# Performance work log

Hardware: AMD Instinct MI355X
Metric: run time of the kernel (lower is better)

The kernel has to match this reference:

```python
import jax, jax.numpy as jnp
import numpy as np

DIM = 180; HEADS = 6; WS = 8; CONV_SCALE = 0.01
B = 4; H = 256; W = 256

def _rpi(ws):
    coords = np.stack(np.meshgrid(np.arange(ws), np.arange(ws), indexing='ij')).reshape(2, -1)
    rel = (coords[:, :, None] - coords[:, None, :]).transpose(1, 2, 0)
    rel[:, :, 0] += ws - 1; rel[:, :, 1] += ws - 1
    rel[:, :, 0] *= 2 * ws - 1
    return rel.sum(-1)  # (ws*ws, ws*ws)

def setup_inputs():
    ks = jax.random.split(jax.random.key(0), 10)
    d = DIM
    n = lambda i, shape: jax.random.normal(ks[i], shape, jnp.float32) * 0.02
    return {
        'x': jax.random.normal(ks[0], (B, H * W, d), jnp.float32),
        'ln1_g': jnp.ones((d,), jnp.float32), 'ln1_b': jnp.zeros((d,), jnp.float32),
        'qkv_w': n(1, (3 * d, d)), 'qkv_b': jnp.zeros((3 * d,), jnp.float32),
        'bias_table': n(2, ((2 * WS - 1) ** 2, HEADS)),
        'proj_w': n(3, (d, d)), 'proj_b': jnp.zeros((d,), jnp.float32),
        'cab_w1': n(4, (d // 3, d, 3, 3)), 'cab_b1': jnp.zeros((d // 3,), jnp.float32),
        'cab_w2': n(5, (d, d // 3, 3, 3)), 'cab_b2': jnp.zeros((d,), jnp.float32),
        'ca_w1': n(6, (d // 30, d, 1, 1)), 'ca_b1': jnp.zeros((d // 30,), jnp.float32),
        'ca_w2': n(7, (d, d // 30, 1, 1)), 'ca_b2': jnp.zeros((d,), jnp.float32),
        'ln2_g': jnp.ones((d,), jnp.float32), 'ln2_b': jnp.zeros((d,), jnp.float32),
        'fc1_w': n(8, (4 * d, d)), 'fc1_b': jnp.zeros((4 * d,), jnp.float32),
        'fc2_w': n(9, (d, 4 * d)), 'fc2_b': jnp.zeros((d,), jnp.float32),
        'rpi': jnp.asarray(_rpi(WS), jnp.int32),
        'h': H, 'w': W,
    }

def _ln(x, g, b, eps=1e-5):
    m = x.mean(-1, keepdims=True)
    v = ((x - m) ** 2).mean(-1, keepdims=True)
    return (x - m) / jnp.sqrt(v + eps) * g + b

def _conv(x, w, b, pad):
    y = jax.lax.conv_general_dilated(x, w, (1, 1), [(pad, pad), (pad, pad)],
                                     dimension_numbers=('NCHW', 'OIHW', 'NCHW'))
    return y + b[None, :, None, None]

def _hab(x, ln1_g, ln1_b, qkv_w, qkv_b, bias_table, proj_w, proj_b,
         cab_w1, cab_b1, cab_w2, cab_b2, ca_w1, ca_b1, ca_w2, ca_b2,
         ln2_g, ln2_b, fc1_w, fc1_b, fc2_w, fc2_b, rpi, h, w):
    b, _, c = x.shape
    ws, heads = WS, HEADS
    hd = c // heads
    shortcut = x
    xn = _ln(x, ln1_g, ln1_b).reshape(b, h, w, c)
    # --- CAB conv branch ---
    xc = xn.transpose(0, 3, 1, 2)  # NCHW
    y = jax.nn.gelu(_conv(xc, cab_w1, cab_b1, 1), approximate=False)
    y = _conv(y, cab_w2, cab_b2, 1)
    a = y.mean((2, 3), keepdims=True)  # adaptive avg pool to 1x1
    a = jax.nn.relu(_conv(a, ca_w1, ca_b1, 0))
    a = jax.nn.sigmoid(_conv(a, ca_w2, ca_b2, 0))
    conv_x = (y * a).transpose(0, 2, 3, 1).reshape(b, h * w, c)
    # --- window attention (shift_size = 0, no mask) ---
    nwin_tok = ws * ws
    xw = xn.reshape(b, h // ws, ws, w // ws, ws, c).transpose(0, 1, 3, 2, 4, 5).reshape(-1, nwin_tok, c)
    qkv = (xw @ qkv_w.T + qkv_b).reshape(-1, nwin_tok, 3, heads, hd).transpose(2, 0, 3, 1, 4)
    q, k, v = qkv[0] * (hd ** -0.5), qkv[1], qkv[2]
    attn = jnp.einsum('whnd,whmd->whnm', q, k)  # (nW*b, heads, n, n)
    bias = bias_table[rpi.reshape(-1)].reshape(nwin_tok, nwin_tok, heads).transpose(2, 0, 1)
    attn = jax.nn.softmax(attn + bias[None], axis=-1)
    out = jnp.einsum('whnm,whmd->whnd', attn, v).transpose(0, 2, 1, 3).reshape(-1, nwin_tok, c)
    out = out @ proj_w.T + proj_b
    attn_x = out.reshape(b, h // ws, w // ws, ws, ws, c).transpose(0, 1, 3, 2, 4, 5).reshape(b, h * w, c)
    x = shortcut + attn_x + conv_x * CONV_SCALE
    x = x + (jax.nn.gelu(_ln(x, ln2_g, ln2_b) @ fc1_w.T + fc1_b, approximate=False) @ fc2_w.T + fc2_b)
    return x

def reference(x, ln1_g, ln1_b, qkv_w, qkv_b, bias_table, proj_w, proj_b,
              cab_w1, cab_b1, cab_w2, cab_b2, ca_w1, ca_b1, ca_w2, ca_b2,
              ln2_g, ln2_b, fc1_w, fc1_b, fc2_w, fc2_b, rpi, h, w):
    return _hab(x, ln1_g, ln1_b, qkv_w, qkv_b, bias_table, proj_w, proj_b,
                cab_w1, cab_b1, cab_w2, cab_b2, ca_w1, ca_b1, ca_w2, ca_b2,
                ln2_g, ln2_b, fc1_w, fc1_b, fc2_w, fc2_b, rpi, h, w)
```

## Files before the change

kernel.cpp:

```cpp
#include <hip/hip_runtime.h>
#include <hip/hip_bf16.h>

typedef __hip_bfloat16 bf16;
typedef __attribute__((ext_vector_type(8))) short short8v;
typedef __attribute__((ext_vector_type(4))) float float4v;

#define N_TOK (4 * 65536)
#define IMG 256

__device__ __forceinline__ float wave_reduce_add(float v) {
#pragma unroll
  for (int m = 32; m > 0; m >>= 1) v += __shfl_xor(v, m, 64);
  return v;
}

__device__ __forceinline__ float gelu_f(float v) {
  return 0.5f * v * (1.f + erff(v * 0.70710678118654752f));
}

__device__ __forceinline__ size_t frag_idx(long row, int k) {
  return ((((row >> 6) * 24) + (k >> 3)) << 9) + ((long)(row & 63) << 3) + (k & 7);
}


__global__ void k_zero(float* __restrict__ p, int n) {
  int i = blockIdx.x * 256 + threadIdx.x;
  if (i < n) p[i] = 0.f;
}

__global__ void k_pack_qkv_b(const float* __restrict__ w, bf16* __restrict__ B) {
  int e = blockIdx.x * 256 + threadIdx.x;
  if (e >= 34 * 6 * 64) return;
  int lane = e & 63, kb = (e >> 6) % 6, nt = e / (6 * 64);
  int n = nt * 16 + (lane & 15);
  int kbase = kb * 32 + (lane >> 4) * 8;
  bf16* out = B + (size_t)e * 8;
#pragma unroll
  for (int j = 0; j < 8; j++) {
    int k = kbase + j;
    float v = 0.f;
    if (n < 540 && k < 180) {
      int hh = n / 90, r = n % 90, mat = r / 30, d = r % 30;
      int o = mat * 180 + hh * 30 + d;
      float s = (mat == 0) ? 0.18257418583505537f : 1.f;
      v = w[o * 180 + k] * s;
    }
    out[j] = __float2bfloat16(v);
  }
}

__global__ void k_pack_qkv_bias(const float* __restrict__ b, float* __restrict__ bt) {
  int n = blockIdx.x * 256 + threadIdx.x;
  if (n >= 544) return;
  float v = 0.f;
  if (n < 540) {
    int hh = n / 90, r = n % 90, mat = r / 30, d = r % 30;
    int o = mat * 180 + hh * 30 + d;
    float s = (mat == 0) ? 0.18257418583505537f : 1.f;
    v = b[o] * s;
  }
  bt[n] = v;
}

__global__ void k_pack_proj_b(const float* __restrict__ w, bf16* __restrict__ B) {
  int e = blockIdx.x * 256 + threadIdx.x;
  if (e >= 12 * 6 * 64) return;
  int lane = e & 63, kb = (e >> 6) % 6, nt = e / (6 * 64);
  int n = nt * 16 + (lane & 15);
  int kbase = kb * 32 + (lane >> 4) * 8;
  bf16* out = B + (size_t)e * 8;
#pragma unroll
  for (int j = 0; j < 8; j++) {
    int k = kbase + j;
    out[j] = __float2bfloat16((n < 180 && k < 180) ? w[n * 180 + k] : 0.f);
  }
}

__global__ void k_pack_fc1_b(const float* __restrict__ w, bf16* __restrict__ B) {
  int e = blockIdx.x * 256 + threadIdx.x;
  if (e >= 46 * 6 * 64) return;
  int lane = e & 63, kb = (e >> 6) % 6, nt = e / (6 * 64);
  int n = nt * 16 + (lane & 15);
  int kbase = kb * 32 + (lane >> 4) * 8;
  bf16* out = B + (size_t)e * 8;
#pragma unroll
  for (int j = 0; j < 8; j++) {
    int k = kbase + j;
    out[j] = __float2bfloat16((n < 720 && k < 180) ? w[n * 180 + k] : 0.f);
  }
}

__global__ void k_pack_fc1_bias(const float* __restrict__ b, float* __restrict__ bt) {
  int n = blockIdx.x * 256 + threadIdx.x;
  if (n >= 736) return;
  bt[n] = (n < 720) ? b[n] : 0.f;
}

__global__ void k_pack_fc2_b(const float* __restrict__ w, bf16* __restrict__ B) {
  int e = blockIdx.x * 256 + threadIdx.x;
  if (e >= 12 * 23 * 64) return;
  int lane = e & 63, kb = (e >> 6) % 23, nt = e / (23 * 64);
  int n = nt * 16 + (lane & 15);
  int kbase = kb * 32 + (lane >> 4) * 8;
  bf16* out = B + (size_t)e * 8;
#pragma unroll
  for (int j = 0; j < 8; j++) {
    int k = kbase + j;
    out[j] = __float2bfloat16((n < 180 && k < 720) ? w[n * 720 + k] : 0.f);
  }
}

__global__ void k_pack_conv1_b(const float* __restrict__ w, bf16* __restrict__ B) {
  int e = blockIdx.x * 256 + threadIdx.x;
  if (e >= 9 * 6 * 4 * 64) return;
  int lane = e & 63;
  int t = e >> 6;
  int nt = t & 3;
  int t2 = t >> 2;
  int dx = t2 % 3;
  int t3 = t2 / 3;
  int kb = t3 % 6, dy = t3 / 6;
  int n = nt * 16 + (lane & 15);
  int kbase = kb * 32 + (lane >> 4) * 8;
  bf16* out = B + (size_t)e * 8;
#pragma unroll
  for (int j = 0; j < 8; j++) {
    int k = kbase + j;
    float v = (n < 60 && k < 180) ? w[((n * 180 + k) * 3 + dy) * 3 + dx] : 0.f;
    out[j] = __float2bfloat16(v);
  }
}

__global__ void k_pack_conv2_b(const float* __restrict__ w, bf16* __restrict__ B) {
  int e = blockIdx.x * 256 + threadIdx.x;
  if (e >= 9 * 2 * 12 * 64) return;
  int lane = e & 63;
  int t = e >> 6;
  int nt = t % 12;
  int t2 = t / 12;
  int dx = t2 % 3;
  int t3 = t2 / 3;
  int kb = t3 & 1, dy = t3 >> 1;
  int n = nt * 16 + (lane & 15);
  int kbase = kb * 32 + (lane >> 4) * 8;
  bf16* out = B + (size_t)e * 8;
#pragma unroll
  for (int j = 0; j < 8; j++) {
    int k = kbase + j;
    float v = (n < 180 && k < 60) ? w[((n * 60 + k) * 3 + dy) * 3 + dx] : 0.f;
    out[j] = __float2bfloat16(v);
  }
}


__global__ __launch_bounds__(256) void k_ln1(const float* __restrict__ x,
                                             const float* __restrict__ gw,
                                             const float* __restrict__ bw,
                                             bf16* __restrict__ xnf) {
  int wv = threadIdx.x >> 6, lane = threadIdx.x & 63;
  long row = (long)blockIdx.x * 4 + wv;
  const float* xr = x + row * 180;
  float v0 = xr[lane];
  float v1 = xr[lane + 64];
  float v2 = (lane < 52) ? xr[lane + 128] : 0.f;
  float s = wave_reduce_add(v0 + v1 + v2);
  float ss = wave_reduce_add(v0 * v0 + v1 * v1 + v2 * v2);
  float mean = s * (1.f / 180.f);
  float rstd = rsqrtf(ss * (1.f / 180.f) - mean * mean + 1e-5f);
  bf16* base = xnf + (((row >> 6) * 24) << 9) + ((long)(row & 63) << 3);
  int ch = lane >> 3, j = lane & 7;
  base[((size_t)ch << 9) + j] =
      __float2bfloat16((v0 - mean) * rstd * gw[lane] + bw[lane]);
  base[((size_t)(ch + 8) << 9) + j] =
      __float2bfloat16((v1 - mean) * rstd * gw[lane + 64] + bw[lane + 64]);
  float v3 = (lane < 52) ? ((v2 - mean) * rstd * gw[lane + 128] + bw[lane + 128]) : 0.f;
  base[((size_t)(ch + 16) << 9) + j] = __float2bfloat16(v3);
}


__global__ __launch_bounds__(256) void k_conv1_mfma(const bf16* __restrict__ xnf,
                                                    const bf16* __restrict__ Bc1,
                                                    const float* __restrict__ b1,
                                                    bf16* __restrict__ y60f) {
  __shared__ bf16 Ls[3 * 12 * 66 * 8];
  int tid = threadIdx.x;
  int bid = blockIdx.x;
  int b = bid >> 10, rem = bid & 1023, iy = rem >> 2, xb = rem & 3;
  int ix0 = xb << 6;
  long ibase = (long)b * 65536;
  int lane = tid & 63, wv = tid >> 6;
  int m = lane & 15, q = lane >> 4;
  float4v acc[4];
#pragma unroll
  for (int nt = 0; nt < 4; nt++) acc[nt] = (float4v){0.f, 0.f, 0.f, 0.f};
  const short8v* Bp = (const short8v*)Bc1;
  for (int half = 0; half < 2; half++) {
    for (int idx = tid; idx < 3 * 12 * 66; idx += 256) {
      int px = idx % 66;
      int t2 = idx / 66;
      int chb = t2 % 12, r = t2 / 12;
      int iy2 = iy - 1 + r, ix = ix0 - 1 + px;
      uint4 v = make_uint4(0u, 0u, 0u, 0u);
      if (iy2 >= 0 && iy2 < IMG && ix >= 0 && ix < IMG) {
        long tok = ibase + iy2 * IMG + ix;
        v = *(const uint4*)(xnf + ((tok >> 6) * 24 + half * 12 + chb) * 512 +
                            (tok & 63) * 8);
      }
      *(uint4*)(Ls + (size_t)idx * 8) = v;
    }
    __syncthreads();
#pragma unroll
    for (int kbl = 0; kbl < 3; kbl++) {
      int kb = half * 3 + kbl;
#pragma unroll
      for (int dy = 0; dy < 3; dy++) {
        const short8v* ab =
            (const short8v*)Ls + ((dy * 12 + kbl * 4 + q) * 66 + wv * 16 + m);
#pragma unroll
        for (int dx = 0; dx < 3; dx++) {
          short8v a = ab[dx];
          const short8v* bp = Bp + (size_t)(((dy * 6 + kb) * 3 + dx) * 4) * 64 + lane;
#pragma unroll
          for (int nt = 0; nt < 4; nt++)
            acc[nt] = __builtin_amdgcn_mfma_f32_16x16x32_bf16(a, bp[nt * 64], acc[nt], 0, 0, 0);
        }
      }
    }
    __syncthreads();
  }
  bf16* outb = y60f + (size_t)bid * 4096;
#pragma unroll
  for (int nt = 0; nt < 4; nt++) {
    int n = nt * 16 + m;
    float bias = (n < 60) ? b1[n] : 0.f;
#pragma unroll
    for (int reg = 0; reg < 4; reg++) {
      int p = wv * 16 + q * 4 + reg;
      float v = (n < 60) ? gelu_f(acc[nt][reg] + bias) : 0.f;
      outb[((n >> 3) << 9) + (p << 3) + (n & 7)] = __float2bfloat16(v);
    }
  }
}


__global__ __launch_bounds__(256) void k_conv2_mfma(const bf16* __restrict__ y60f,
                                                    const bf16* __restrict__ Bc2,
                                                    const float* __restrict__ b2,
                                                    bf16* __restrict__ y180f,
                                                    float* __restrict__ chsum) {
  __shared__ bf16 Ls[3 * 8 * 66 * 8];
  int tid = threadIdx.x;
  int bid = blockIdx.x;
  int b = bid >> 10, rem = bid & 1023, iy = rem >> 2, xb = rem & 3;
  int ix0 = xb << 6;
  long ibase = (long)b * 65536;
  for (int idx = tid; idx < 3 * 8 * 66; idx += 256) {
    int px = idx % 66;
    int t2 = idx / 66;
    int chb = t2 % 8, r = t2 / 8;
    int iy2 = iy - 1 + r, ix = ix0 - 1 + px;
    uint4 v = make_uint4(0u, 0u, 0u, 0u);
    if (iy2 >= 0 && iy2 < IMG && ix >= 0 && ix < IMG) {
      long tok = ibase + iy2 * IMG + ix;
      v = *(const uint4*)(y60f + ((tok >> 6) * 8 + chb) * 512 + (tok & 63) * 8);
    }
    *(uint4*)(Ls + (size_t)idx * 8) = v;
  }
  __syncthreads();
  int lane = tid & 63, wv = tid >> 6;
  int m = lane & 15, q = lane >> 4;
  float4v acc[12];
#pragma unroll
  for (int nt = 0; nt < 12; nt++) acc[nt] = (float4v){0.f, 0.f, 0.f, 0.f};
  const short8v* Bp = (const short8v*)Bc2;
#pragma unroll
  for (int dy = 0; dy < 3; dy++) {
#pragma unroll
    for (int kb = 0; kb < 2; kb++) {
      const short8v* ab =
          (const short8v*)Ls + ((dy * 8 + kb * 4 + q) * 66 + wv * 16 + m);
#pragma unroll
      for (int dx = 0; dx < 3; dx++) {
        short8v a = ab[dx];
        const short8v* bp = Bp + (size_t)(((dy * 2 + kb) * 3 + dx) * 12) * 64 + lane;
#pragma unroll
        for (int nt = 0; nt < 12; nt++)
          acc[nt] = __builtin_amdgcn_mfma_f32_16x16x32_bf16(a, bp[nt * 64], acc[nt], 0, 0, 0);
      }
    }
  }
  float csum[12];
  bf16* outb = y180f + (size_t)bid * 12288;
#pragma unroll
  for (int nt = 0; nt < 12; nt++) {
    int n = nt * 16 + m;
    float bias = (n < 180) ? b2[n] : 0.f;
    float s = 0.f;
#pragma unroll
    for (int reg = 0; reg < 4; reg++) {
      float v = acc[nt][reg] + bias;
      s += v;
      int p = wv * 16 + q * 4 + reg;
      if (n < 180) outb[((n >> 3) << 9) + (p << 3) + (n & 7)] = __float2bfloat16(v);
    }
    s += __shfl_xor(s, 16, 64);
    s += __shfl_xor(s, 32, 64);
    csum[nt] = s;
  }
  __syncthreads();
  float* red = (float*)Ls;
  if (q == 0) {
#pragma unroll
    for (int nt = 0; nt < 12; nt++) red[wv * 192 + nt * 16 + m] = csum[nt];
  }
  __syncthreads();
  if (tid < 180) {
    float tot = red[tid] + red[192 + tid] + red[384 + tid] + red[576 + tid];
    atomicAdd(&chsum[b * 180 + tid], tot);
  }
}


__global__ __launch_bounds__(192) void k_se(const float* __restrict__ cs,
                                            const float* __restrict__ w1,
                                            const float* __restrict__ b1,
                                            const float* __restrict__ w2,
                                            const float* __restrict__ b2,
                                            float* __restrict__ a_se) {
  __shared__ float m[180];
  __shared__ float hid[6];
  int b = blockIdx.x, t = threadIdx.x;
  if (t < 180) m[t] = cs[b * 180 + t] * (1.f / 65536.f);
  __syncthreads();
  if (t < 6) {
    float s = b1[t];
    for (int c = 0; c < 180; c++) s += m[c] * w1[t * 180 + c];
    hid[t] = fmaxf(s, 0.f);
  }
  __syncthreads();
  if (t < 180) {
    float s = b2[t];
#pragma unroll
    for (int j = 0; j < 6; j++) s += hid[j] * w2[t * 6 + j];
    a_se[b * 180 + t] = 1.f / (1.f + __expf(-s));
  }
}


__global__ __launch_bounds__(256) void k_qkv_mfma(const bf16* __restrict__ xnf,
                                                  const bf16* __restrict__ Bq,
                                                  const float* __restrict__ btq,
                                                  bf16* __restrict__ qkvb) {
  __shared__ bf16 As[24 * 64 * 8];
  int tid = threadIdx.x;
  const uint4* src = (const uint4*)(xnf + (size_t)blockIdx.x * 12288);
  uint4* dst = (uint4*)As;
#pragma unroll
  for (int it = 0; it < 6; it++) dst[it * 256 + tid] = src[it * 256 + tid];
  __syncthreads();
  int lane = tid & 63, wv = tid >> 6;
  int m = lane & 15, q = lane >> 4;
  long row0 = (long)blockIdx.x * 64 + wv * 16;
  const short8v* Ap = (const short8v*)As;
  const short8v* Bp = (const short8v*)Bq;
  for (int nt = 0; nt < 34; nt += 2) {
    float4v acc0 = {0.f, 0.f, 0.f, 0.f}, acc1 = {0.f, 0.f, 0.f, 0.f};
#pragma unroll
    for (int kb = 0; kb < 6; kb++) {
      short8v a = Ap[(kb * 4 + q) * 64 + wv * 16 + m];
      short8v b0 = Bp[(nt * 6 + kb) * 64 + lane];
      short8v b1 = Bp[((nt + 1) * 6 + kb) * 64 + lane];
      acc0 = __builtin_amdgcn_mfma_f32_16x16x32_bf16(a, b0, acc0, 0, 0, 0);
      acc1 = __builtin_amdgcn_mfma_f32_16x16x32_bf16(a, b1, acc1, 0, 0, 0);
    }
    int n0 = nt * 16 + m, n1 = n0 + 16;
    float bb0 = btq[n0], bb1 = btq[n1];
#pragma unroll
    for (int reg = 0; reg < 4; reg++) {
      long rw = row0 + q * 4 + reg;
      qkvb[rw * 544 + n0] = __float2bfloat16(acc0[reg] + bb0);
      qkvb[rw * 544 + n1] = __float2bfloat16(acc1[reg] + bb1);
    }
  }
}


__global__ __launch_bounds__(256) void k_attn(const bf16* __restrict__ qkvb,
                                              const float* __restrict__ btab,
                                              const int* __restrict__ rpi,
                                              bf16* __restrict__ attnf) {
  __shared__ float qkvh[90 * 65];
  __shared__ float sT[64 * 65];
  int h = blockIdx.y;
  int bid = blockIdx.x;
  int b = bid >> 10, rem = bid & 1023, wi = rem >> 5, wj = rem & 31;
  long ibase = (long)b * 65536;
  if (h == 0 && threadIdx.x < 64) {
    int n = threadIdx.x;
    long g = ibase + (wi * 8 + (n >> 3)) * IMG + wj * 8 + (n & 7);
    bf16* bp = attnf + (((g >> 6) * 24) << 9) + ((long)(g & 63) << 3);
    *(uint2*)(bp + (22 << 9) + 4) = make_uint2(0u, 0u);
    *(uint4*)(bp + (23 << 9)) = make_uint4(0u, 0u, 0u, 0u);
  }
  for (int idx = threadIdx.x; idx < 64 * 90; idx += 256) {
    int t = idx / 90, r = idx % 90;
    long g = ibase + (wi * 8 + (t >> 3)) * IMG + wj * 8 + (t & 7);
    qkvh[r * 65 + t] = __bfloat162float(qkvb[g * 544 + h * 90 + r]);
  }
  __syncthreads();
  {
    int m = threadIdx.x & 63, ng = threadIdx.x >> 6;
    int n0 = ng * 16;
    float acc[16];
#pragma unroll
    for (int j = 0; j < 16; j++) acc[j] = 0.f;
    for (int d = 0; d < 30; d++) {
      float kv = qkvh[(30 + d) * 65 + m];
      const float* qp = qkvh + d * 65 + n0;
#pragma unroll
      for (int j = 0; j < 16; j++) acc[j] += kv * qp[j];
    }
#pragma unroll
    for (int j = 0; j < 16; j++) {
      int n = n0 + j;
      sT[m * 65 + n] = acc[j] + btab[rpi[n * 64 + m] * 6 + h];
    }
  }
  __syncthreads();
  if (threadIdx.x < 64) {
    int n = threadIdx.x;
    float mx = -1e30f;
    for (int m2 = 0; m2 < 64; m2++) mx = fmaxf(mx, sT[m2 * 65 + n]);
    float s = 0.f;
    for (int m2 = 0; m2 < 64; m2++) {
      float e = __expf(sT[m2 * 65 + n] - mx);
      sT[m2 * 65 + n] = e;
      s += e;
    }
    float inv = 1.f / s;
    for (int m2 = 0; m2 < 64; m2++) sT[m2 * 65 + n] *= inv;
  }
  __syncthreads();
  for (int it = threadIdx.x; it < 120; it += 256) {
    int d = it % 30, ng = it / 30;
    int n0 = ng * 16;
    float acc[16];
#pragma unroll
    for (int j = 0; j < 16; j++) acc[j] = 0.f;
    for (int m2 = 0; m2 < 64; m2++) {
      float vv = qkvh[(60 + d) * 65 + m2];
      const float* pp = sT + m2 * 65 + n0;
#pragma unroll
      for (int j = 0; j < 16; j++) acc[j] += vv * pp[j];
    }
    int k = h * 30 + d;
#pragma unroll
    for (int j = 0; j < 16; j++) {
      int n = n0 + j;
      long g = ibase + (wi * 8 + (n >> 3)) * IMG + wj * 8 + (n & 7);
      attnf[frag_idx(g, k)] = __float2bfloat16(acc[j]);
    }
  }
}


__global__ __launch_bounds__(256) void k_proj_mfma(const bf16* __restrict__ attnf,
                                                   const bf16* __restrict__ Bp_,
                                                   const float* __restrict__ pb,
                                                   const float* __restrict__ x0,
                                                   const bf16* __restrict__ y180f,
                                                   const float* __restrict__ a_se,
                                                   float* __restrict__ out) {
  __shared__ bf16 As[24 * 64 * 8];
  int tid = threadIdx.x;
  const uint4* src = (const uint4*)(attnf + (size_t)blockIdx.x * 12288);
  uint4* dst = (uint4*)As;
#pragma unroll
  for (int it = 0; it < 6; it++) dst[it * 256 + tid] = src[it * 256 + tid];
  __syncthreads();
  int lane = tid & 63, wv = tid >> 6;
  int m = lane & 15, q = lane >> 4;
  long row0 = (long)blockIdx.x * 64 + wv * 16;
  const short8v* Ap = (const short8v*)As;
  const short8v* Bpp = (const short8v*)Bp_;
  for (int nt = 0; nt < 12; nt += 2) {
    float4v acc0 = {0.f, 0.f, 0.f, 0.f}, acc1 = {0.f, 0.f, 0.f, 0.f};
#pragma unroll
    for (int kb = 0; kb < 6; kb++) {
      short8v a = Ap[(kb * 4 + q) * 64 + wv * 16 + m];
      short8v b0 = Bpp[(nt * 6 + kb) * 64 + lane];
      short8v b1 = Bpp[((nt + 1) * 6 + kb) * 64 + lane];
      acc0 = __builtin_amdgcn_mfma_f32_16x16x32_bf16(a, b0, acc0, 0, 0, 0);
      acc1 = __builtin_amdgcn_mfma_f32_16x16x32_bf16(a, b1, acc1, 0, 0, 0);
    }
    int n0 = nt * 16 + m, n1 = n0 + 16;
    float pb0 = pb[n0];
    float pb1 = (n1 < 180) ? pb[n1] : 0.f;
#pragma unroll
    for (int reg = 0; reg < 4; reg++) {
      long rw = row0 + q * 4 + reg;
      int bidx = (int)(rw >> 16);
      long gi0 = rw * 180 + n0;
      out[gi0] = x0[gi0] + acc0[reg] + pb0 +
                 __bfloat162float(y180f[frag_idx(rw, n0)]) * a_se[bidx * 180 + n0] * 0.01f;
      if (n1 < 180) {
        long gi1 = rw * 180 + n1;
        out[gi1] = x0[gi1] + acc1[reg] + pb1 +
                   __bfloat162float(y180f[frag_idx(rw, n1)]) * a_se[bidx * 180 + n1] * 0.01f;
      }
    }
  }
}


__global__ __launch_bounds__(512, 4) void k_mlp_mfma(float* __restrict__ xio,
                                                     const float* __restrict__ gw,
                                                     const float* __restrict__ bw,
                                                     const bf16* __restrict__ B1,
                                                     const float* __restrict__ b1t,
                                                     const bf16* __restrict__ B2,
                                                     const float* __restrict__ fc2b) {
  __shared__ bf16 Axs[32 * 200];
  __shared__ bf16 Hs[32 * 744];
  int tid = threadIdx.x, lane = tid & 63, wv = tid >> 6;
  long row0 = (long)blockIdx.x * 32;
#pragma unroll
  for (int rr = 0; rr < 4; rr++) {
    int r = wv * 4 + rr;
    const float* xr = xio + (row0 + r) * 180;
    float v0 = xr[lane], v1 = xr[lane + 64];
    float v2 = (lane < 52) ? xr[lane + 128] : 0.f;
    float s = wave_reduce_add(v0 + v1 + v2);
    float ss = wave_reduce_add(v0 * v0 + v1 * v1 + v2 * v2);
    float mean = s * (1.f / 180.f);
    float rstd = rsqrtf(ss * (1.f / 180.f) - mean * mean + 1e-5f);
    bf16* ar = Axs + r * 200;
    ar[lane] = __float2bfloat16((v0 - mean) * rstd * gw[lane] + bw[lane]);
    ar[lane + 64] = __float2bfloat16((v1 - mean) * rstd * gw[lane + 64] + bw[lane + 64]);
    float v3 = (lane < 52) ? ((v2 - mean) * rstd * gw[lane + 128] + bw[lane + 128]) : 0.f;
    ar[lane + 128] = __float2bfloat16(v3);
  }
  __syncthreads();
  int m = lane & 15, q = lane >> 4, mh = wv & 1, ng = wv >> 1;
  int rA = mh * 16 + m;
  for (int i = 0; i < 12; i += 2) {
    int nt0 = ng * 12 + i;
    if (nt0 >= 46) break;
    bool two = (nt0 + 1) < 46;
    float4v acc0 = {0.f, 0.f, 0.f, 0.f}, acc1 = {0.f, 0.f, 0.f, 0.f};
#pragma unroll
    for (int kb = 0; kb < 6; kb++) {
      short8v a = *(const short8v*)(Axs + rA * 200 + kb * 32 + q * 8);
      short8v b0 = ((const short8v*)B1)[(nt0 * 6 + kb) * 64 + lane];
      acc0 = __builtin_amdgcn_mfma_f32_16x16x32_bf16(a, b0, acc0, 0, 0, 0);
      if (two) {
        short8v b1 = ((const short8v*)B1)[((nt0 + 1) * 6 + kb) * 64 + lane];
        acc1 = __builtin_amdgcn_mfma_f32_16x16x32_bf16(a, b1, acc1, 0, 0, 0);
      }
    }
    int n0 = nt0 * 16 + m;
    float bb0 = b1t[n0];
    float bb1 = two ? b1t[n0 + 16] : 0.f;
#pragma unroll
    for (int reg = 0; reg < 4; reg++) {
      int r = mh * 16 + q * 4 + reg;
      Hs[r * 744 + n0] = __float2bfloat16(gelu_f(acc0[reg] + bb0));
      if (two) Hs[r * 744 + n0 + 16] = __float2bfloat16(gelu_f(acc1[reg] + bb1));
    }
  }
  __syncthreads();
  for (int i = 0; i < 3; i += 2) {
    int nt0 = ng * 3 + i;
    bool two = (i + 1) < 3;
    float4v acc0 = {0.f, 0.f, 0.f, 0.f}, acc1 = {0.f, 0.f, 0.f, 0.f};
    for (int kb = 0; kb < 23; kb++) {
      short8v a = *(const short8v*)(Hs + rA * 744 + kb * 32 + q * 8);
      short8v b0 = ((const short8v*)B2)[(nt0 * 23 + kb) * 64 + lane];
      acc0 = __builtin_amdgcn_mfma_f32_16x16x32_bf16(a, b0, acc0, 0, 0, 0);
      if (two) {
        short8v b1 = ((const short8v*)B2)[((nt0 + 1) * 23 + kb) * 64 + lane];
        acc1 = __builtin_amdgcn_mfma_f32_16x16x32_bf16(a, b1, acc1, 0, 0, 0);
      }
    }
    int n0 = nt0 * 16 + m, n1 = n0 + 16;
#pragma unroll
    for (int reg = 0; reg < 4; reg++) {
      long rw = row0 + mh * 16 + q * 4 + reg;
      if (n0 < 180) xio[rw * 180 + n0] += acc0[reg] + fc2b[n0];
      if (two && n1 < 180) xio[rw * 180 + n1] += acc1[reg] + fc2b[n1];
    }
  }
}


extern "C" void kernel_launch(void* const* d_in, const int* in_sizes, int n_in,
                              void* d_out, int out_size, void* d_ws, size_t ws_size,
                              hipStream_t stream) {
  const float* x = (const float*)d_in[0];
  const float* ln1g = (const float*)d_in[1];
  const float* ln1b = (const float*)d_in[2];
  const float* qkvw = (const float*)d_in[3];
  const float* qkvbias = (const float*)d_in[4];
  const float* btab = (const float*)d_in[5];
  const float* projw = (const float*)d_in[6];
  const float* projb = (const float*)d_in[7];
  const float* cw1 = (const float*)d_in[8];
  const float* cb1 = (const float*)d_in[9];
  const float* cw2 = (const float*)d_in[10];
  const float* cb2 = (const float*)d_in[11];
  const float* caw1 = (const float*)d_in[12];
  const float* cab1 = (const float*)d_in[13];
  const float* caw2 = (const float*)d_in[14];
  const float* cab2 = (const float*)d_in[15];
  const float* ln2g = (const float*)d_in[16];
  const float* ln2b = (const float*)d_in[17];
  const float* fc1w = (const float*)d_in[18];
  const float* fc1b = (const float*)d_in[19];
  const float* fc2w = (const float*)d_in[20];
  const float* fc2b = (const float*)d_in[21];
  const int* rpi = (const int*)d_in[22];
  float* out = (float*)d_out;

  size_t off = 0;
  char* wsb = (char*)d_ws;
  auto alloc = [&](size_t bytes) -> char* {
    char* p = wsb + off;
    off = (off + bytes + 255) & ~(size_t)255;
    return p;
  };
  bf16* xnf = (bf16*)alloc((size_t)N_TOK * 192 * 2);
  bf16* y60f = (bf16*)alloc((size_t)N_TOK * 64 * 2);
  bf16* y180f = (bf16*)alloc((size_t)N_TOK * 192 * 2);
  bf16* qkvb = (bf16*)alloc((size_t)N_TOK * 544 * 2);
  bf16* Bq = (bf16*)alloc(34 * 6 * 64 * 8 * 2);
  float* btq = (float*)alloc(544 * 4);
  bf16* Bp = (bf16*)alloc(12 * 6 * 64 * 8 * 2);
  bf16* B1 = (bf16*)alloc(46 * 6 * 64 * 8 * 2);
  float* b1t = (float*)alloc(736 * 4);
  bf16* B2 = (bf16*)alloc(12 * 23 * 64 * 8 * 2);
  bf16* Bc1 = (bf16*)alloc(9 * 6 * 4 * 64 * 8 * 2);
  bf16* Bc2 = (bf16*)alloc(9 * 2 * 12 * 64 * 8 * 2);
  float* chsum = (float*)alloc(720 * 4);
  float* a_se = (float*)alloc(720 * 4);
  if (off > ws_size) return;
  bf16* attnf = xnf;

  k_zero<<<3, 256, 0, stream>>>(chsum, 720);
  k_pack_qkv_b<<<51, 256, 0, stream>>>(qkvw, Bq);
  k_pack_qkv_bias<<<3, 256, 0, stream>>>(qkvbias, btq);
  k_pack_proj_b<<<18, 256, 0, stream>>>(projw, Bp);
  k_pack_fc1_b<<<69, 256, 0, stream>>>(fc1w, B1);
  k_pack_fc1_bias<<<3, 256, 0, stream>>>(fc1b, b1t);
  k_pack_fc2_b<<<69, 256, 0, stream>>>(fc2w, B2);
  k_pack_conv1_b<<<54, 256, 0, stream>>>(cw1, Bc1);
  k_pack_conv2_b<<<54, 256, 0, stream>>>(cw2, Bc2);

  k_ln1<<<65536, 256, 0, stream>>>(x, ln1g, ln1b, xnf);
  k_conv1_mfma<<<4096, 256, 0, stream>>>(xnf, Bc1, cb1, y60f);
  k_conv2_mfma<<<4096, 256, 0, stream>>>(y60f, Bc2, cb2, y180f, chsum);
  k_se<<<4, 192, 0, stream>>>(chsum, caw1, cab1, caw2, cab2, a_se);
  k_qkv_mfma<<<4096, 256, 0, stream>>>(xnf, Bq, btq, qkvb);
  k_attn<<<dim3(4096, 6), 256, 0, stream>>>(qkvb, btab, rpi, attnf);
  k_proj_mfma<<<4096, 256, 0, stream>>>(attnf, Bp, projb, x, y180f, a_se, out);
  k_mlp_mfma<<<8192, 512, 0, stream>>>(out, ln2g, ln2b, B1, b1t, B2, fc2b);
}
```

Measured before the change: 2.320 ms.

## Rewrite window attention with bf16 MFMA and pad per-head QKV to 32

```diff
diff --git a/kernel.cpp b/kernel.cpp
--- a/kernel.cpp
+++ b/kernel.cpp
@@ -30,17 +30,17 @@
 
 __global__ void k_pack_qkv_b(const float* __restrict__ w, bf16* __restrict__ B) {
   int e = blockIdx.x * 256 + threadIdx.x;
-  if (e >= 34 * 6 * 64) return;
+  if (e >= 36 * 6 * 64) return;
   int lane = e & 63, kb = (e >> 6) % 6, nt = e / (6 * 64);
   int n = nt * 16 + (lane & 15);
   int kbase = kb * 32 + (lane >> 4) * 8;
   bf16* out = B + (size_t)e * 8;
+  int hh = n / 96, rr = n % 96, mat = rr / 32, d = rr % 32;
 #pragma unroll
   for (int j = 0; j < 8; j++) {
     int k = kbase + j;
     float v = 0.f;
-    if (n < 540 && k < 180) {
-      int hh = n / 90, r = n % 90, mat = r / 30, d = r % 30;
+    if (d < 30 && k < 180) {
       int o = mat * 180 + hh * 30 + d;
       float s = (mat == 0) ? 0.18257418583505537f : 1.f;
       v = w[o * 180 + k] * s;
@@ -51,15 +51,23 @@
 
 __global__ void k_pack_qkv_bias(const float* __restrict__ b, float* __restrict__ bt) {
   int n = blockIdx.x * 256 + threadIdx.x;
-  if (n >= 544) return;
+  if (n >= 576) return;
+  int hh = n / 96, rr = n % 96, mat = rr / 32, d = rr % 32;
   float v = 0.f;
-  if (n < 540) {
-    int hh = n / 90, r = n % 90, mat = r / 30, d = r % 30;
+  if (d < 30) {
     int o = mat * 180 + hh * 30 + d;
     float s = (mat == 0) ? 0.18257418583505537f : 1.f;
     v = b[o] * s;
   }
   bt[n] = v;
+}
+
+__global__ void k_pack_bias6(const float* __restrict__ btab, const int* __restrict__ rpi,
+                             float* __restrict__ bt6) {
+  int e = blockIdx.x * 256 + threadIdx.x;
+  if (e >= 6 * 4096) return;
+  int h = e >> 12, r = e & 4095;
+  bt6[e] = btab[rpi[r] * 6 + h];
 }
 
 __global__ void k_pack_proj_b(const float* __restrict__ w, bf16* __restrict__ B) {
@@ -363,7 +371,7 @@
   long row0 = (long)blockIdx.x * 64 + wv * 16;
   const short8v* Ap = (const short8v*)As;
   const short8v* Bp = (const short8v*)Bq;
-  for (int nt = 0; nt < 34; nt += 2) {
+  for (int nt = 0; nt < 36; nt += 2) {
     float4v acc0 = {0.f, 0.f, 0.f, 0.f}, acc1 = {0.f, 0.f, 0.f, 0.f};
 #pragma unroll
     for (int kb = 0; kb < 6; kb++) {
@@ -378,89 +386,135 @@
 #pragma unroll
     for (int reg = 0; reg < 4; reg++) {
       long rw = row0 + q * 4 + reg;
-      qkvb[rw * 544 + n0] = __float2bfloat16(acc0[reg] + bb0);
-      qkvb[rw * 544 + n1] = __float2bfloat16(acc1[reg] + bb1);
-    }
-  }
-}
-
-
-__global__ __launch_bounds__(256) void k_attn(const bf16* __restrict__ qkvb,
-                                              const float* __restrict__ btab,
-                                              const int* __restrict__ rpi,
-                                              bf16* __restrict__ attnf) {
-  __shared__ float qkvh[90 * 65];
-  __shared__ float sT[64 * 65];
+      qkvb[rw * 576 + n0] = __float2bfloat16(acc0[reg] + bb0);
+      qkvb[rw * 576 + n1] = __float2bfloat16(acc1[reg] + bb1);
+    }
+  }
+}
+
+
+__global__ __launch_bounds__(64) void k_attn(const bf16* __restrict__ qkvb,
+                                             const float* __restrict__ bt6,
+                                             bf16* __restrict__ attnf) {
+  __shared__ bf16 P_lds[64 * 72];
+  int lane = threadIdx.x;
   int h = blockIdx.y;
   int bid = blockIdx.x;
   int b = bid >> 10, rem = bid & 1023, wi = rem >> 5, wj = rem & 31;
   long ibase = (long)b * 65536;
-  if (h == 0 && threadIdx.x < 64) {
-    int n = threadIdx.x;
-    long g = ibase + (wi * 8 + (n >> 3)) * IMG + wj * 8 + (n & 7);
+  if (h == 0) {
+    long g = ibase + (wi * 8 + (lane >> 3)) * IMG + wj * 8 + (lane & 7);
     bf16* bp = attnf + (((g >> 6) * 24) << 9) + ((long)(g & 63) << 3);
     *(uint2*)(bp + (22 << 9) + 4) = make_uint2(0u, 0u);
     *(uint4*)(bp + (23 << 9)) = make_uint4(0u, 0u, 0u, 0u);
   }
-  for (int idx = threadIdx.x; idx < 64 * 90; idx += 256) {
-    int t = idx / 90, r = idx % 90;
-    long g = ibase + (wi * 8 + (t >> 3)) * IMG + wj * 8 + (t & 7);
-    qkvh[r * 65 + t] = __bfloat162float(qkvb[g * 544 + h * 90 + r]);
-  }
-  __syncthreads();
-  {
-    int m = threadIdx.x & 63, ng = threadIdx.x >> 6;
-    int n0 = ng * 16;
-    float acc[16];
-#pragma unroll
-    for (int j = 0; j < 16; j++) acc[j] = 0.f;
-    for (int d = 0; d < 30; d++) {
-      float kv = qkvh[(30 + d) * 65 + m];
-      const float* qp = qkvh + d * 65 + n0;
-#pragma unroll
-      for (int j = 0; j < 16; j++) acc[j] += kv * qp[j];
-    }
-#pragma unroll
-    for (int j = 0; j < 16; j++) {
-      int n = n0 + j;
-      sT[m * 65 + n] = acc[j] + btab[rpi[n * 64 + m] * 6 + h];
-    }
-  }
-  __syncthreads();
-  if (threadIdx.x < 64) {
-    int n = threadIdx.x;
-    float mx = -1e30f;
-    for (int m2 = 0; m2 < 64; m2++) mx = fmaxf(mx, sT[m2 * 65 + n]);
-    float s = 0.f;
-    for (int m2 = 0; m2 < 64; m2++) {
-      float e = __expf(sT[m2 * 65 + n] - mx);
-      sT[m2 * 65 + n] = e;
-      s += e;
-    }
-    float inv = 1.f / s;
-    for (int m2 = 0; m2 < 64; m2++) sT[m2 * 65 + n] *= inv;
-  }
-  __syncthreads();
-  for (int it = threadIdx.x; it < 120; it += 256) {
-    int d = it % 30, ng = it / 30;
-    int n0 = ng * 16;
-    float acc[16];
-#pragma unroll
-    for (int j = 0; j < 16; j++) acc[j] = 0.f;
-    for (int m2 = 0; m2 < 64; m2++) {
-      float vv = qkvh[(60 + d) * 65 + m2];
-      const float* pp = sT + m2 * 65 + n0;
-#pragma unroll
-      for (int j = 0; j < 16; j++) acc[j] += vv * pp[j];
-    }
-    int k = h * 30 + d;
-#pragma unroll
-    for (int j = 0; j < 16; j++) {
-      int n = n0 + j;
-      long g = ibase + (wi * 8 + (n >> 3)) * IMG + wj * 8 + (n & 7);
-      attnf[frag_idx(g, k)] = __float2bfloat16(acc[j]);
-    }
-  }
+  int ml = lane & 15, q = lane >> 4;
+  long tokr[4];
+#pragma unroll
+  for (int mt = 0; mt < 4; mt++) {
+    int t = mt * 16 + ml;
+    tokr[mt] = ibase + (wi * 8 + (t >> 3)) * IMG + wj * 8 + (t & 7);
+  }
+  short8v aQ[4], bK[4];
+#pragma unroll
+  for (int mt = 0; mt < 4; mt++) {
+    aQ[mt] = *(const short8v*)(qkvb + tokr[mt] * 576 + h * 96 + q * 8);
+    bK[mt] = *(const short8v*)(qkvb + tokr[mt] * 576 + h * 96 + 32 + q * 8);
+  }
+  float4v s[4][4];
+#pragma unroll
+  for (int mt = 0; mt < 4; mt++)
+#pragma unroll
+    for (int nt = 0; nt < 4; nt++)
+      s[mt][nt] = __builtin_amdgcn_mfma_f32_16x16x32_bf16(
+          aQ[mt], bK[nt], (float4v){0.f, 0.f, 0.f, 0.f}, 0, 0, 0);
+  const float* bh = bt6 + h * 4096;
+#pragma unroll
+  for (int mt = 0; mt < 4; mt++)
+#pragma unroll
+    for (int nt = 0; nt < 4; nt++) {
+      int nk = nt * 16 + ml;
+#pragma unroll
+      for (int reg = 0; reg < 4; reg++)
+        s[mt][nt][reg] += bh[(mt * 16 + q * 4 + reg) * 64 + nk];
+    }
+#pragma unroll
+  for (int mt = 0; mt < 4; mt++) {
+#pragma unroll
+    for (int reg = 0; reg < 4; reg++) {
+      float mx = fmaxf(fmaxf(s[mt][0][reg], s[mt][1][reg]),
+                       fmaxf(s[mt][2][reg], s[mt][3][reg]));
+      mx = fmaxf(mx, __shfl_xor(mx, 1, 64));
+      mx = fmaxf(mx, __shfl_xor(mx, 2, 64));
+      mx = fmaxf(mx, __shfl_xor(mx, 4, 64));
+      mx = fmaxf(mx, __shfl_xor(mx, 8, 64));
+      float e0 = __expf(s[mt][0][reg] - mx);
+      float e1 = __expf(s[mt][1][reg] - mx);
+      float e2 = __expf(s[mt][2][reg] - mx);
+      float e3 = __expf(s[mt][3][reg] - mx);
+      float sm = e0 + e1 + e2 + e3;
+      sm += __shfl_xor(sm, 1, 64);
+      sm += __shfl_xor(sm, 2, 64);
+      sm += __shfl_xor(sm, 4, 64);
+      sm += __shfl_xor(sm, 8, 64);
+      float inv = 1.f / sm;
+      s[mt][0][reg] = e0 * inv;
+      s[mt][1][reg] = e1 * inv;
+      s[mt][2][reg] = e2 * inv;
+      s[mt][3][reg] = e3 * inv;
+    }
+  }
+#pragma unroll
+  for (int mt = 0; mt < 4; mt++)
+#pragma unroll
+    for (int reg = 0; reg < 4; reg++) {
+      int mq = mt * 16 + q * 4 + reg;
+#pragma unroll
+      for (int nt = 0; nt < 4; nt++)
+        P_lds[mq * 72 + nt * 16 + ml] = __float2bfloat16(s[mt][nt][reg]);
+    }
+  __syncthreads();
+  float4v o[4][2];
+#pragma unroll
+  for (int mt = 0; mt < 4; mt++)
+#pragma unroll
+    for (int nt = 0; nt < 2; nt++) o[mt][nt] = (float4v){0.f, 0.f, 0.f, 0.f};
+#pragma unroll
+  for (int kb = 0; kb < 2; kb++) {
+    int krow = kb * 4 + q;
+    long tokb = ibase + (wi * 8 + krow) * IMG + wj * 8;
+    short8v bV[2];
+#pragma unroll
+    for (int nt = 0; nt < 2; nt++) {
+      int d = nt * 16 + ml;
+      short8v v;
+#pragma unroll
+      for (int j = 0; j < 8; j++)
+        v[j] = ((const short*)qkvb)[(tokb + j) * 576 + h * 96 + 64 + d];
+      bV[nt] = v;
+    }
+#pragma unroll
+    for (int mt = 0; mt < 4; mt++) {
+      short8v aP = *(const short8v*)(P_lds + (mt * 16 + ml) * 72 + kb * 32 + q * 8);
+#pragma unroll
+      for (int nt = 0; nt < 2; nt++)
+        o[mt][nt] = __builtin_amdgcn_mfma_f32_16x16x32_bf16(aP, bV[nt], o[mt][nt], 0, 0, 0);
+    }
+  }
+#pragma unroll
+  for (int mt = 0; mt < 4; mt++)
+#pragma unroll
+    for (int nt = 0; nt < 2; nt++) {
+      int d = nt * 16 + ml;
+      if (d < 30) {
+#pragma unroll
+        for (int reg = 0; reg < 4; reg++) {
+          int mq = mt * 16 + q * 4 + reg;
+          long g = ibase + (wi * 8 + (mq >> 3)) * IMG + wj * 8 + (mq & 7);
+          attnf[frag_idx(g, h * 30 + d)] = __float2bfloat16(o[mt][nt][reg]);
+        }
+      }
+    }
 }
 
 
@@ -631,23 +685,25 @@
   bf16* xnf = (bf16*)alloc((size_t)N_TOK * 192 * 2);
   bf16* y60f = (bf16*)alloc((size_t)N_TOK * 64 * 2);
   bf16* y180f = (bf16*)alloc((size_t)N_TOK * 192 * 2);
-  bf16* qkvb = (bf16*)alloc((size_t)N_TOK * 544 * 2);
-  bf16* Bq = (bf16*)alloc(34 * 6 * 64 * 8 * 2);
-  float* btq = (float*)alloc(544 * 4);
+  bf16* qkvb = (bf16*)alloc((size_t)N_TOK * 576 * 2);
+  bf16* Bq = (bf16*)alloc(36 * 6 * 64 * 8 * 2);
+  float* btq = (float*)alloc(576 * 4);
   bf16* Bp = (bf16*)alloc(12 * 6 * 64 * 8 * 2);
   bf16* B1 = (bf16*)alloc(46 * 6 * 64 * 8 * 2);
   float* b1t = (float*)alloc(736 * 4);
   bf16* B2 = (bf16*)alloc(12 * 23 * 64 * 8 * 2);
   bf16* Bc1 = (bf16*)alloc(9 * 6 * 4 * 64 * 8 * 2);
   bf16* Bc2 = (bf16*)alloc(9 * 2 * 12 * 64 * 8 * 2);
+  float* bt6 = (float*)alloc(6 * 4096 * 4);
   float* chsum = (float*)alloc(720 * 4);
   float* a_se = (float*)alloc(720 * 4);
   if (off > ws_size) return;
   bf16* attnf = xnf;
 
   k_zero<<<3, 256, 0, stream>>>(chsum, 720);
-  k_pack_qkv_b<<<51, 256, 0, stream>>>(qkvw, Bq);
+  k_pack_qkv_b<<<54, 256, 0, stream>>>(qkvw, Bq);
   k_pack_qkv_bias<<<3, 256, 0, stream>>>(qkvbias, btq);
+  k_pack_bias6<<<96, 256, 0, stream>>>(btab, rpi, bt6);
   k_pack_proj_b<<<18, 256, 0, stream>>>(projw, Bp);
   k_pack_fc1_b<<<69, 256, 0, stream>>>(fc1w, B1);
   k_pack_fc1_bias<<<3, 256, 0, stream>>>(fc1b, b1t);
@@ -660,7 +716,7 @@
   k_conv2_mfma<<<4096, 256, 0, stream>>>(y60f, Bc2, cb2, y180f, chsum);
   k_se<<<4, 192, 0, stream>>>(chsum, caw1, cab1, caw2, cab2, a_se);
   k_qkv_mfma<<<4096, 256, 0, stream>>>(xnf, Bq, btq, qkvb);
-  k_attn<<<dim3(4096, 6), 256, 0, stream>>>(qkvb, btab, rpi, attnf);
+  k_attn<<<dim3(4096, 6), 64, 0, stream>>>(qkvb, bt6, attnf);
   k_proj_mfma<<<4096, 256, 0, stream>>>(attnf, Bp, projb, x, y180f, a_se, out);
   k_mlp_mfma<<<8192, 512, 0, stream>>>(out, ln2g, ln2b, B1, b1t, B2, fc2b);
 }
```

Measured after the change: 1.908 ms. -17.8%, faster.
